# Kernel optimization log

Hardware: AMD Instinct MI355X
Metric: run time of the kernel (lower is better)

## Reference

```python
import jax, jax.numpy as jnp
import numpy as np

B = 4            # num sequences
Q_LEN = 512      # new query tokens per sequence
KV_LEN = 2048    # total kv context per sequence
PAST = KV_LEN - Q_LEN
N_QO, N_KV, HEAD = 32, 8, 128
BS = 16          # page / block size
BLOCKS_PER_SEQ = KV_LEN // BS
NUM_BLOCKS = B * BLOCKS_PER_SEQ


def setup_inputs() -> dict:
    key = jax.random.key(0)
    k1, k2, k3, k4, k5 = jax.random.split(key, 5)
    n_tokens = B * Q_LEN
    query = jax.random.normal(k1, (n_tokens, N_QO * HEAD), dtype=jnp.float32)
    key_t = jax.random.normal(k2, (n_tokens, N_KV * HEAD), dtype=jnp.float32)
    value_t = jax.random.normal(k3, (n_tokens, N_KV * HEAD), dtype=jnp.float32)
    key_cache = jax.random.normal(k4, (NUM_BLOCKS, BS, N_KV, HEAD), dtype=jnp.float32)
    value_cache = jax.random.normal(k5, (NUM_BLOCKS, BS, N_KV, HEAD), dtype=jnp.float32)
    # block tables: a permutation of all blocks (each seq owns disjoint, shuffled pages)
    rng = np.random.default_rng(0)
    bt = rng.permutation(NUM_BLOCKS).reshape(B, BLOCKS_PER_SEQ).astype(np.int32)
    # slot indices (into flattened [num_blocks*block_size] token space) for the new tokens
    pos = np.arange(PAST, KV_LEN)                        # positions of new tokens in each seq
    slots = bt[:, pos // BS] * BS + (pos % BS)           # [B, Q_LEN]
    return {
        'query': query,
        'key': key_t,
        'value': value_t,
        'key_cache': key_cache,
        'value_cache': value_cache,
        'block_tables': jnp.asarray(bt),
        'new_cache_slots': jnp.asarray(slots.reshape(-1), dtype=jnp.int32),
    }


def reference(query, key, value, key_cache, value_cache, block_tables, new_cache_slots):
    n_tokens = query.shape[0]
    num_blocks, bs, n_kv, d = key_cache.shape
    b, blocks_per_seq = block_tables.shape
    q_len = n_tokens // b
    kv_len = blocks_per_seq * bs
    n_qo = query.shape[1] // d
    g = n_qo // n_kv  # GQA group size

    q = query.reshape(b, q_len, n_qo, d).astype(jnp.float32)
    k_new = key.reshape(n_tokens, n_kv, d)
    v_new = value.reshape(n_tokens, n_kv, d)

    # write new k/v into the paged cache at their slots (set_kv_cache)
    kc = key_cache.reshape(num_blocks * bs, n_kv, d).at[new_cache_slots].set(k_new)
    vc = value_cache.reshape(num_blocks * bs, n_kv, d).at[new_cache_slots].set(v_new)

    # per-sequence paged gather: token t of seq i lives at block_tables[i, t//bs]*bs + t%bs
    tok_idx = (block_tables[:, :, None] * bs + jnp.arange(bs, dtype=block_tables.dtype)).reshape(b, kv_len)
    k = kc[tok_idx].astype(jnp.float32)  # [b, kv_len, n_kv, d]
    v = vc[tok_idx].astype(jnp.float32)

    # GQA: query head (h*g + j) attends with kv head h (== repeat_interleave on kv heads)
    qg = q.reshape(b, q_len, n_kv, g, d)
    sm_scale = 1.0 / jnp.sqrt(jnp.float32(d))
    scores = jnp.einsum('bqhgd,bkhd->bhgqk', qg, k) * sm_scale  # [b, n_kv, g, q, kv]

    # causal mask with offset: mask where k_idx - q_idx > kv_len - q_len
    q_idx = jnp.arange(q_len)
    k_idx = jnp.arange(kv_len)
    mask = (k_idx[None, :] - q_idx[:, None]) > (kv_len - q_len)  # [q, kv]
    scores = jnp.where(mask, -jnp.inf, scores)

    p = jax.nn.softmax(scores, axis=-1)
    o = jnp.einsum('bhgqk,bkhd->bqhgd', p, v)  # [b, q, n_kv, g, d]
    return o.reshape(n_tokens, n_qo * d).astype(query.dtype)
```

## Files before the change

### kernel.cpp

```cpp
#include <hip/hip_runtime.h>
#include <hip/hip_bf16.h>

#define BQ    4
#define QL    512
#define KVL   2048
#define PASTN 1536
#define NKV   8
#define DH    128
#define BPS   128

typedef __bf16 bf16x8 __attribute__((ext_vector_type(8)));
typedef float  f32x4  __attribute__((ext_vector_type(4)));
typedef float  f32x16 __attribute__((ext_vector_type(16)));

#if __has_builtin(__builtin_amdgcn_exp2f)
#define EXP2F(x) __builtin_amdgcn_exp2f(x)
#else
#define EXP2F(x) exp2f(x)
#endif

__device__ __forceinline__ unsigned short f32_to_bf16(float f) {
    unsigned u = __builtin_bit_cast(unsigned, f);
    u += 0x7fffu + ((u >> 16) & 1u);
    return (unsigned short)(u >> 16);
}

__device__ __forceinline__ unsigned pk_bf16(float a, float b) {
    return (unsigned)f32_to_bf16(a) | ((unsigned)f32_to_bf16(b) << 16);
}

__device__ __forceinline__ unsigned pk_trunc(float lo, float hi) {
    return __builtin_amdgcn_perm(__builtin_bit_cast(unsigned, hi),
                                 __builtin_bit_cast(unsigned, lo), 0x07060302u);
}

__device__ __forceinline__ void load_lds16(const unsigned short* g, unsigned short* l) {
    __builtin_amdgcn_global_load_lds(
        (const __attribute__((address_space(1))) void*)g,
        (__attribute__((address_space(3))) void*)l, 16, 0, 0);
}

__device__ __forceinline__ void swap32(unsigned &x, unsigned &y) {
    asm("v_permlane32_swap_b32 %0, %1" : "+v"(x), "+v"(y));
}

__device__ __forceinline__ void lacc_add(float &L, unsigned p) {
    L += __builtin_bit_cast(float, p << 16);
    L += __builtin_bit_cast(float, p & 0xffff0000u);
}

#define VLS 132
__global__ __launch_bounds__(256) void gather_kv_kernel(
    const float* __restrict__ key, const float* __restrict__ key_cache,
    const float* __restrict__ value, const float* __restrict__ value_cache,
    const int* __restrict__ bt, unsigned short* __restrict__ Kb,
    unsigned short* __restrict__ VTb)
{
  __shared__ unsigned short Vl[64 * VLS];
  const int bid = blockIdx.x;
  if (bid < 8192) {
    const int gidx = bid * 256 + threadIdx.x;
    const int d  = (gidx & 31) * 4;
    const int p  = (gidx >> 5) & (KVL - 1);
    const int bh = gidx >> 16;
    const int hh = bh & 7;
    const int bb = bh >> 3;
    const float* src;
    if (p < PASTN) {
      const int blk = bt[bb * BPS + (p >> 4)];
      src = key_cache + (size_t)((blk * 16 + (p & 15)) * 8 + hh) * DH + d;
    } else {
      src = key + (size_t)((bb * QL + (p - PASTN)) * 8 + hh) * DH + d;
    }
    const float4 v = *(const float4*)src;
    uint2 o;
    o.x = pk_bf16(v.x, v.y);
    o.y = pk_bf16(v.z, v.w);
    *(uint2*)(Kb + ((size_t)bh * KVL + p) * DH + d) = o;
  } else {
    const int vbid = bid - 8192;
    const int t   = vbid & 31;
    const int hh  = (vbid >> 5) & 7;
    const int bb  = vbid >> 8;
    const int tid = threadIdx.x;
    const int dl  = (tid & 31) * 4;
    const int p0  = tid >> 5;
#pragma unroll
    for (int it = 0; it < 8; ++it) {
      const int pl = p0 + it * 8;
      const int gp = t * 64 + pl;
      const float* src;
      if (gp < PASTN) {
        const int blk = bt[bb * BPS + (gp >> 4)];
        src = value_cache + (size_t)((blk * 16 + (gp & 15)) * 8 + hh) * DH + dl;
      } else {
        src = value + (size_t)((bb * QL + (gp - PASTN)) * 8 + hh) * DH + dl;
      }
      const float4 v = *(const float4*)src;
      uint2 o;
      o.x = pk_bf16(v.x, v.y);
      o.y = pk_bf16(v.z, v.w);
      *(uint2*)&Vl[pl * VLS + dl] = o;
    }
    __syncthreads();
#pragma unroll
    for (int it = 0; it < 4; ++it) {
      const int slot = it * 256 + tid;
      const int d    = slot >> 3;
      const int kv0  = (slot & 7) * 8;
      unsigned rr[4];
#pragma unroll
      for (int i = 0; i < 4; ++i) {
        const unsigned lo = Vl[(kv0 + 2 * i) * VLS + d];
        const unsigned hi = Vl[(kv0 + 2 * i + 1) * VLS + d];
        rr[i] = lo | (hi << 16);
      }
      *(uint4*)(VTb + ((size_t)(bb * 8 + hh) * DH + d) * KVL + t * 64 + kv0) =
          make_uint4(rr[0], rr[1], rr[2], rr[3]);
    }
  }
}

__global__ __launch_bounds__(256, 2) void attn_kernel(
    const float* __restrict__ query,
    const unsigned short* __restrict__ Kb,
    const unsigned short* __restrict__ VTb,
    float* __restrict__ out)
{
  __shared__ unsigned short Klds[2][64 * 128];
  __shared__ unsigned short Vtlds[2][128 * 64];

  const int tid  = threadIdx.x;
  const int w    = tid >> 6;
  const int lane = tid & 63;
  const int cq   = lane & 31;
  const int hi   = lane >> 5;
  const int xk   = cq & 7;

  const int gid = blockIdx.x;
  const int qb  = gid >> 5;
  const int bh  = gid & 31;
  const int b   = bh >> 3;
  const int h   = bh & 7;
  const int q0  = qb * 32;
  const int n_tiles = ((PASTN + q0 + 31) >> 6) + 1;
  const int lim = PASTN + q0 - 64 * (n_tiles - 1);
  const int hq  = h * 4 + w;

  const int kx = lane >> 4;
  const int ku = lane & 15;
  const unsigned short* kgp[4];
#pragma unroll
  for (int i = 0; i < 4; ++i) {
    const int row = 16 * w + 4 * i + kx;
    kgp[i] = Kb + ((size_t)bh * KVL + row) * DH + (ku ^ (row & 7)) * 8;
  }
  const int vx = lane >> 3;
  const int vu = lane & 7;
  const unsigned short* vgp[4];
#pragma unroll
  for (int i = 0; i < 4; ++i) {
    const int row = 32 * w + 8 * i + vx;
    vgp[i] = VTb + ((size_t)bh * DH + row) * KVL + (vu ^ vx) * 8;
  }

  auto issue_tile = [&](int buf) {
#pragma unroll
    for (int i = 0; i < 4; ++i)
      load_lds16(kgp[i], &Klds[buf][2048 * w + 512 * i]);
#pragma unroll
    for (int i = 0; i < 4; ++i)
      load_lds16(vgp[i], &Vtlds[buf][2048 * w + 512 * i]);
#pragma unroll
    for (int i = 0; i < 4; ++i) { kgp[i] += 64 * DH; vgp[i] += 64; }
  };

  issue_tile(0);

  const float qscale = 0.08838834764831845f * 1.4426950408889634f;

  bf16x8 qf[8];
  {
    const float* qp = query + (size_t)(b * QL + q0 + cq) * 4096 + hq * DH + 8 * hi;
#pragma unroll
    for (int ks = 0; ks < 8; ++ks) {
      float4 x = *(const float4*)(qp + 16 * ks);
      float4 y = *(const float4*)(qp + 16 * ks + 4);
      uint4 u;
      u.x = pk_bf16(x.x * qscale, x.y * qscale);
      u.y = pk_bf16(x.z * qscale, x.w * qscale);
      u.z = pk_bf16(y.x * qscale, y.y * qscale);
      u.w = pk_bf16(y.z * qscale, y.w * qscale);
      qf[ks] = __builtin_bit_cast(bf16x8, u);
    }
  }

  f32x16 Oacc[4];
#pragma unroll
  for (int dt = 0; dt < 4; ++dt)
#pragma unroll
    for (int i = 0; i < 16; ++i) Oacc[dt][i] = 0.f;
  float Lp[4] = {0.f, 0.f, 0.f, 0.f};

  for (int t = 0; t < n_tiles; ++t) {
    const int buf = t & 1;
    __syncthreads();
    if (t + 1 < n_tiles) issue_tile(buf ^ 1);

    f32x16 S0, S1;
#pragma unroll
    for (int i = 0; i < 16; ++i) { S0[i] = 0.f; S1[i] = 0.f; }
    __builtin_amdgcn_s_setprio(1);
#pragma unroll
    for (int ks = 0; ks < 8; ++ks) {
      const bf16x8 a0 = __builtin_bit_cast(bf16x8,
          *(const uint4*)&Klds[buf][(cq)      * 128 + 8 * ((2 * ks + hi) ^ xk)]);
      const bf16x8 a1 = __builtin_bit_cast(bf16x8,
          *(const uint4*)&Klds[buf][(32 + cq) * 128 + 8 * ((2 * ks + hi) ^ xk)]);
      S0 = __builtin_amdgcn_mfma_f32_32x32x16_bf16(a0, qf[ks], S0, 0, 0, 0);
      S1 = __builtin_amdgcn_mfma_f32_32x32x16_bf16(a1, qf[ks], S1, 0, 0, 0);
    }
    __builtin_amdgcn_s_setprio(0);

    uint4 vfr[4][4];
#pragma unroll
    for (int ss = 0; ss < 4; ++ss)
#pragma unroll
      for (int dt = 0; dt < 4; ++dt)
        vfr[ss][dt] = *(const uint4*)&Vtlds[buf][(32 * dt + cq) * 64 + 8 * ((2 * ss + hi) ^ xk)];

    if (t == n_tiles - 1) {
#pragma unroll
      for (int reg = 0; reg < 16; ++reg) {
        const int rr = (reg & 3) + 8 * (reg >> 2) + 4 * hi;
        if (rr - cq > lim)      S0[reg] = -1e30f;
        if (32 + rr - cq > lim) S1[reg] = -1e30f;
      }
    }

#pragma unroll
    for (int step = 0; step < 4; ++step) {
      const f32x16 S = (step < 2) ? S0 : S1;
      const int s = step & 1;
      unsigned p01 = pk_trunc(EXP2F(S[8 * s + 0]), EXP2F(S[8 * s + 1]));
      unsigned p23 = pk_trunc(EXP2F(S[8 * s + 2]), EXP2F(S[8 * s + 3]));
      unsigned q01 = pk_trunc(EXP2F(S[8 * s + 4]), EXP2F(S[8 * s + 5]));
      unsigned q23 = pk_trunc(EXP2F(S[8 * s + 6]), EXP2F(S[8 * s + 7]));
      lacc_add(Lp[step], p01); lacc_add(Lp[step], p23);
      lacc_add(Lp[step], q01); lacc_add(Lp[step], q23);
      swap32(p01, q01);
      swap32(p23, q23);
      uint4 u; u.x = p01; u.y = p23; u.z = q01; u.w = q23;
      const bf16x8 pf = __builtin_bit_cast(bf16x8, u);
      __builtin_amdgcn_s_setprio(1);
#pragma unroll
      for (int dt = 0; dt < 4; ++dt) {
        const bf16x8 vf = __builtin_bit_cast(bf16x8, vfr[step][dt]);
        Oacc[dt] = __builtin_amdgcn_mfma_f32_32x32x16_bf16(vf, pf, Oacc[dt], 0, 0, 0);
      }
      __builtin_amdgcn_s_setprio(0);
    }
  }

  {
    const float Ls = (Lp[0] + Lp[1]) + (Lp[2] + Lp[3]);
    const float other = __shfl_xor(Ls, 32, 64);
    const float inv = 1.0f / (Ls + other);
    float* op = out + (size_t)(b * QL + q0 + cq) * 4096 + hq * DH + 4 * hi;
#pragma unroll
    for (int dt = 0; dt < 4; ++dt) {
#pragma unroll
      for (int rq = 0; rq < 4; ++rq) {
        float4 o4;
        o4.x = Oacc[dt][4 * rq + 0] * inv;
        o4.y = Oacc[dt][4 * rq + 1] * inv;
        o4.z = Oacc[dt][4 * rq + 2] * inv;
        o4.w = Oacc[dt][4 * rq + 3] * inv;
        *(float4*)(op + 32 * dt + 8 * rq) = o4;
      }
    }
  }
}

extern "C" void kernel_launch(void* const* d_in, const int* in_sizes, int n_in,
                              void* d_out, int out_size, void* d_ws, size_t ws_size,
                              hipStream_t stream) {
  const float* query = (const float*)d_in[0];
  const float* key   = (const float*)d_in[1];
  const float* value = (const float*)d_in[2];
  const float* kc    = (const float*)d_in[3];
  const float* vc    = (const float*)d_in[4];
  const int*   bt    = (const int*)d_in[5];
  float* out = (float*)d_out;

  unsigned short* Kb  = (unsigned short*)d_ws;
  unsigned short* VTb = Kb + (size_t)32 * KVL * DH;

  gather_kv_kernel<<<9216, 256, 0, stream>>>(key, kc, value, vc, bt, Kb, VTb);
  attn_kernel<<<512, 256, 0, stream>>>(query, Kb, VTb, out);
}
```

Baseline: 228.4 us.

## Split KV loop across two wave groups per block with LDS output reduction

The attention block grows from 4 to 8 waves. Two groups of four waves each handle alternating 32-row KV sub-tiles with their own double-buffered LDS regions. Partial O accumulators and row sums are then combined through shared memory before normalisation. This cuts the serial KV loop length per wave and raises occupancy, at the cost of a larger LDS footprint, an extra reduction pass, and smaller MFMA work per step. The V staging stride in the gather kernel also changes, with narrower stores, to alter LDS bank behaviour.

```diff
diff --git a/kernel.cpp b/kernel.cpp
--- a/kernel.cpp
+++ b/kernel.cpp
@@ -49,7 +49,7 @@
     L += __builtin_bit_cast(float, p & 0xffff0000u);
 }
 
-#define VLS 132
+#define VLS 130
 __global__ __launch_bounds__(256) void gather_kv_kernel(
     const float* __restrict__ key, const float* __restrict__ key_cache,
     const float* __restrict__ value, const float* __restrict__ value_cache,
@@ -97,10 +97,9 @@
         src = value + (size_t)((bb * QL + (gp - PASTN)) * 8 + hh) * DH + dl;
       }
       const float4 v = *(const float4*)src;
-      uint2 o;
-      o.x = pk_bf16(v.x, v.y);
-      o.y = pk_bf16(v.z, v.w);
-      *(uint2*)&Vl[pl * VLS + dl] = o;
+      unsigned short* dst = &Vl[pl * VLS + dl];
+      *(unsigned*)(dst)     = pk_bf16(v.x, v.y);
+      *(unsigned*)(dst + 2) = pk_bf16(v.z, v.w);
     }
     __syncthreads();
 #pragma unroll
@@ -121,21 +120,23 @@
   }
 }
 
-__global__ __launch_bounds__(256, 2) void attn_kernel(
+__global__ __launch_bounds__(512, 4) void attn_kernel(
     const float* __restrict__ query,
     const unsigned short* __restrict__ Kb,
     const unsigned short* __restrict__ VTb,
     float* __restrict__ out)
 {
-  __shared__ unsigned short Klds[2][64 * 128];
-  __shared__ unsigned short Vtlds[2][128 * 64];
+  __shared__ unsigned short SM[33280];
 
   const int tid  = threadIdx.x;
   const int w    = tid >> 6;
+  const int grp  = w >> 2;
+  const int wh   = w & 3;
   const int lane = tid & 63;
   const int cq   = lane & 31;
   const int hi   = lane >> 5;
   const int xk   = cq & 7;
+  const int xk3  = cq & 3;
 
   const int gid = blockIdx.x;
   const int qb  = gid >> 5;
@@ -143,36 +144,37 @@
   const int b   = bh >> 3;
   const int h   = bh & 7;
   const int q0  = qb * 32;
-  const int n_tiles = ((PASTN + q0 + 31) >> 6) + 1;
-  const int lim = PASTN + q0 - 64 * (n_tiles - 1);
-  const int hq  = h * 4 + w;
+  const int M     = (PASTN >> 5) + 1 + qb;
+  const int ITmax = (M + 1) >> 1;
+  const int mask_it = (((M - 1) & 1) == grp) ? ((M - 1 - grp) >> 1) : -1;
+  const int hq  = h * 4 + wh;
 
   const int kx = lane >> 4;
   const int ku = lane & 15;
-  const unsigned short* kgp[4];
-#pragma unroll
-  for (int i = 0; i < 4; ++i) {
-    const int row = 16 * w + 4 * i + kx;
-    kgp[i] = Kb + ((size_t)bh * KVL + row) * DH + (ku ^ (row & 7)) * 8;
-  }
-  const int vx = lane >> 3;
-  const int vu = lane & 7;
-  const unsigned short* vgp[4];
-#pragma unroll
-  for (int i = 0; i < 4; ++i) {
-    const int row = 32 * w + 8 * i + vx;
-    vgp[i] = VTb + ((size_t)bh * DH + row) * KVL + (vu ^ vx) * 8;
+  const unsigned short* kgp[2];
+#pragma unroll
+  for (int i = 0; i < 2; ++i) {
+    const int rl = 8 * wh + 4 * i + kx;
+    kgp[i] = Kb + ((size_t)bh * KVL + grp * 32 + rl) * DH + (ku ^ (rl & 7)) * 8;
+  }
+  const int vr4 = lane >> 2;
+  const int vu  = lane & 3;
+  const unsigned short* vgp[2];
+#pragma unroll
+  for (int i = 0; i < 2; ++i) {
+    const int rl = 32 * wh + 16 * i + vr4;
+    vgp[i] = VTb + ((size_t)bh * DH + rl) * KVL + grp * 32 + (vu ^ (vr4 & 3)) * 8;
   }
 
   auto issue_tile = [&](int buf) {
-#pragma unroll
-    for (int i = 0; i < 4; ++i)
-      load_lds16(kgp[i], &Klds[buf][2048 * w + 512 * i]);
-#pragma unroll
-    for (int i = 0; i < 4; ++i)
-      load_lds16(vgp[i], &Vtlds[buf][2048 * w + 512 * i]);
-#pragma unroll
-    for (int i = 0; i < 4; ++i) { kgp[i] += 64 * DH; vgp[i] += 64; }
+    unsigned short* kb = &SM[(grp * 2 + buf) * 4096 + wh * 1024];
+    load_lds16(kgp[0], kb);
+    load_lds16(kgp[1], kb + 512);
+    unsigned short* vb = kb + 16384;
+    load_lds16(vgp[0], vb);
+    load_lds16(vgp[1], vb + 512);
+    kgp[0] += 64 * DH; kgp[1] += 64 * DH;
+    vgp[0] += 64;      vgp[1] += 64;
   };
 
   issue_tile(0);
@@ -200,82 +202,90 @@
   for (int dt = 0; dt < 4; ++dt)
 #pragma unroll
     for (int i = 0; i < 16; ++i) Oacc[dt][i] = 0.f;
-  float Lp[4] = {0.f, 0.f, 0.f, 0.f};
-
-  for (int t = 0; t < n_tiles; ++t) {
-    const int buf = t & 1;
+  float Ls = 0.f;
+
+  for (int it = 0; it < ITmax; ++it) {
+    const int buf = it & 1;
     __syncthreads();
-    if (t + 1 < n_tiles) issue_tile(buf ^ 1);
-
-    f32x16 S0, S1;
-#pragma unroll
-    for (int i = 0; i < 16; ++i) { S0[i] = 0.f; S1[i] = 0.f; }
-    __builtin_amdgcn_s_setprio(1);
-#pragma unroll
-    for (int ks = 0; ks < 8; ++ks) {
-      const bf16x8 a0 = __builtin_bit_cast(bf16x8,
-          *(const uint4*)&Klds[buf][(cq)      * 128 + 8 * ((2 * ks + hi) ^ xk)]);
-      const bf16x8 a1 = __builtin_bit_cast(bf16x8,
-          *(const uint4*)&Klds[buf][(32 + cq) * 128 + 8 * ((2 * ks + hi) ^ xk)]);
-      S0 = __builtin_amdgcn_mfma_f32_32x32x16_bf16(a0, qf[ks], S0, 0, 0, 0);
-      S1 = __builtin_amdgcn_mfma_f32_32x32x16_bf16(a1, qf[ks], S1, 0, 0, 0);
-    }
-    __builtin_amdgcn_s_setprio(0);
-
-    uint4 vfr[4][4];
-#pragma unroll
-    for (int ss = 0; ss < 4; ++ss)
-#pragma unroll
-      for (int dt = 0; dt < 4; ++dt)
-        vfr[ss][dt] = *(const uint4*)&Vtlds[buf][(32 * dt + cq) * 64 + 8 * ((2 * ss + hi) ^ xk)];
-
-    if (t == n_tiles - 1) {
-#pragma unroll
-      for (int reg = 0; reg < 16; ++reg) {
-        const int rr = (reg & 3) + 8 * (reg >> 2) + 4 * hi;
-        if (rr - cq > lim)      S0[reg] = -1e30f;
-        if (32 + rr - cq > lim) S1[reg] = -1e30f;
-      }
-    }
-
-#pragma unroll
-    for (int step = 0; step < 4; ++step) {
-      const f32x16 S = (step < 2) ? S0 : S1;
-      const int s = step & 1;
-      unsigned p01 = pk_trunc(EXP2F(S[8 * s + 0]), EXP2F(S[8 * s + 1]));
-      unsigned p23 = pk_trunc(EXP2F(S[8 * s + 2]), EXP2F(S[8 * s + 3]));
-      unsigned q01 = pk_trunc(EXP2F(S[8 * s + 4]), EXP2F(S[8 * s + 5]));
-      unsigned q23 = pk_trunc(EXP2F(S[8 * s + 6]), EXP2F(S[8 * s + 7]));
-      lacc_add(Lp[step], p01); lacc_add(Lp[step], p23);
-      lacc_add(Lp[step], q01); lacc_add(Lp[step], q23);
-      swap32(p01, q01);
-      swap32(p23, q23);
-      uint4 u; u.x = p01; u.y = p23; u.z = q01; u.w = q23;
-      const bf16x8 pf = __builtin_bit_cast(bf16x8, u);
-      __builtin_amdgcn_s_setprio(1);
-#pragma unroll
-      for (int dt = 0; dt < 4; ++dt) {
-        const bf16x8 vf = __builtin_bit_cast(bf16x8, vfr[step][dt]);
-        Oacc[dt] = __builtin_amdgcn_mfma_f32_32x32x16_bf16(vf, pf, Oacc[dt], 0, 0, 0);
-      }
-      __builtin_amdgcn_s_setprio(0);
-    }
-  }
-
-  {
-    const float Ls = (Lp[0] + Lp[1]) + (Lp[2] + Lp[3]);
-    const float other = __shfl_xor(Ls, 32, 64);
-    const float inv = 1.0f / (Ls + other);
+    if (2 * (it + 1) + grp < M) issue_tile(buf ^ 1);
+    if (2 * it + grp < M) {
+      const unsigned short* Kr = &SM[(grp * 2 + buf) * 4096];
+      const unsigned short* Vr = Kr + 16384;
+
+      f32x16 S;
+#pragma unroll
+      for (int i = 0; i < 16; ++i) S[i] = 0.f;
+#pragma unroll
+      for (int ks = 0; ks < 8; ++ks) {
+        const bf16x8 af = __builtin_bit_cast(bf16x8,
+            *(const uint4*)&Kr[cq * 128 + 8 * ((2 * ks + hi) ^ xk)]);
+        S = __builtin_amdgcn_mfma_f32_32x32x16_bf16(af, qf[ks], S, 0, 0, 0);
+      }
+
+      if (it == mask_it) {
+#pragma unroll
+        for (int reg = 0; reg < 16; ++reg) {
+          const int rr = (reg & 3) + 8 * (reg >> 2) + 4 * hi;
+          if (rr > cq) S[reg] = -1e30f;
+        }
+      }
+
+#pragma unroll
+      for (int s = 0; s < 2; ++s) {
+        unsigned p01 = pk_trunc(EXP2F(S[8 * s + 0]), EXP2F(S[8 * s + 1]));
+        unsigned p23 = pk_trunc(EXP2F(S[8 * s + 2]), EXP2F(S[8 * s + 3]));
+        unsigned q01 = pk_trunc(EXP2F(S[8 * s + 4]), EXP2F(S[8 * s + 5]));
+        unsigned q23 = pk_trunc(EXP2F(S[8 * s + 6]), EXP2F(S[8 * s + 7]));
+        lacc_add(Ls, p01); lacc_add(Ls, p23);
+        lacc_add(Ls, q01); lacc_add(Ls, q23);
+        swap32(p01, q01);
+        swap32(p23, q23);
+        uint4 u; u.x = p01; u.y = p23; u.z = q01; u.w = q23;
+        const bf16x8 pf = __builtin_bit_cast(bf16x8, u);
+#pragma unroll
+        for (int dt = 0; dt < 4; ++dt) {
+          const bf16x8 vf = __builtin_bit_cast(bf16x8,
+              *(const uint4*)&Vr[(32 * dt + cq) * 32 + 8 * ((2 * s + hi) ^ xk3)]);
+          Oacc[dt] = __builtin_amdgcn_mfma_f32_32x32x16_bf16(vf, pf, Oacc[dt], 0, 0, 0);
+        }
+      }
+    }
+  }
+
+  __syncthreads();
+  float* Ob = (float*)&SM[0];
+  float* Lb = (float*)&SM[32768];
+  const int l15 = lane & 15;
+  if (grp == 1) {
+    Lb[wh * 64 + lane] = Ls;
+    float* myO = Ob + wh * 4096 + lane * 64;
+#pragma unroll
+    for (int dt = 0; dt < 4; ++dt)
+#pragma unroll
+      for (int rq = 0; rq < 4; ++rq) {
+        f32x4 c;
+        c[0] = Oacc[dt][4 * rq + 0]; c[1] = Oacc[dt][4 * rq + 1];
+        c[2] = Oacc[dt][4 * rq + 2]; c[3] = Oacc[dt][4 * rq + 3];
+        *(f32x4*)(myO + ((dt * 4 + rq) ^ l15) * 4) = c;
+      }
+  }
+  __syncthreads();
+  if (grp == 0) {
+    const float Lsum  = Ls + Lb[wh * 64 + lane];
+    const float other = __shfl_xor(Lsum, 32, 64);
+    const float inv   = 1.0f / (Lsum + other);
+    const float* myO = Ob + wh * 4096 + lane * 64;
     float* op = out + (size_t)(b * QL + q0 + cq) * 4096 + hq * DH + 4 * hi;
 #pragma unroll
     for (int dt = 0; dt < 4; ++dt) {
 #pragma unroll
       for (int rq = 0; rq < 4; ++rq) {
+        const f32x4 c = *(const f32x4*)(myO + ((dt * 4 + rq) ^ l15) * 4);
         float4 o4;
-        o4.x = Oacc[dt][4 * rq + 0] * inv;
-        o4.y = Oacc[dt][4 * rq + 1] * inv;
-        o4.z = Oacc[dt][4 * rq + 2] * inv;
-        o4.w = Oacc[dt][4 * rq + 3] * inv;
+        o4.x = (Oacc[dt][4 * rq + 0] + c[0]) * inv;
+        o4.y = (Oacc[dt][4 * rq + 1] + c[1]) * inv;
+        o4.z = (Oacc[dt][4 * rq + 2] + c[2]) * inv;
+        o4.w = (Oacc[dt][4 * rq + 3] + c[3]) * inv;
         *(float4*)(op + 32 * dt + 8 * rq) = o4;
       }
     }
@@ -297,5 +307,5 @@
   unsigned short* VTb = Kb + (size_t)32 * KVL * DH;
 
   gather_kv_kernel<<<9216, 256, 0, stream>>>(key, kc, value, vc, bt, Kb, VTb);
-  attn_kernel<<<512, 256, 0, stream>>>(query, Kb, VTb, out);
-}
+  attn_kernel<<<512, 512, 0, stream>>>(query, Kb, VTb, out);
+}
```

After: 303.2 us. 1.33x slower.
